# Performance work log

Hardware: AMD Instinct MI355X
Metric: run time of the kernel (lower is better)

## Reference

```python
import jax, jax.numpy as jnp
import numpy as np

NUM_HEADS = 8
WS = 7          # window size (hardcoded in source)
SR = 4          # sr_ratio
EPS = 1e-5


def _win_partition(t, ws, H, W):
    # t: [B, h, N, d] -> [B*h*nW, ws*ws, d]
    B, h, N, d = t.shape
    t = t.reshape(B * h, H // ws, ws, W // ws, ws, d)
    t = t.transpose(0, 1, 3, 2, 4, 5)
    return t.reshape(-1, ws * ws, d)


def _win_reverse(w, ws, H, W, h):
    # w: [B*h*nW, ws*ws, d] -> [B, H*W, h*d]
    d = w.shape[-1]
    Bh = w.shape[0] // ((H // ws) * (W // ws))
    x = w.reshape(Bh, H // ws, W // ws, ws, ws, d).transpose(0, 1, 3, 2, 4, 5)
    x = x.reshape(Bh // h, h, H, W, d).transpose(0, 2, 3, 1, 4)
    return x.reshape(Bh // h, H * W, h * d)


def setup_inputs() -> dict:
    key = jax.random.key(0)
    B, H, W, C = 32, 56, 56, 256
    N = H * W
    ks = jax.random.split(key, 10)
    s = lambda k, shp: jax.random.normal(k, shp, dtype=jnp.float32) * 0.02
    return {
        "x": jax.random.normal(ks[0], (B, N, C), dtype=jnp.float32),
        "lepe_lin_w": s(ks[1], (C, C)), "lepe_lin_b": jnp.zeros((C,), jnp.float32),
        "lepe_conv_w": s(ks[2], (3, 3, 1, C)), "lepe_conv_b": jnp.zeros((C,), jnp.float32),
        "sr_w": s(ks[3], (SR, SR, C, C)), "sr_b": jnp.zeros((C,), jnp.float32),
        "norm_g": jnp.ones((C,), jnp.float32), "norm_b": jnp.zeros((C,), jnp.float32),
        "q1_w": s(ks[4], (C, C // 2)), "kv1_w": s(ks[5], (C, C)),
        "q2_w": s(ks[6], (C, C // 2)), "kv2_w": s(ks[7], (C, C)),
        "proj_w": s(ks[8], (C, C)), "proj_b": jnp.zeros((C,), jnp.float32),
        "H": H, "W": W,
    }


def reference(x, lepe_lin_w, lepe_lin_b, lepe_conv_w, lepe_conv_b, sr_w, sr_b,
              norm_g, norm_b, q1_w, kv1_w, q2_w, kv2_w, proj_w, proj_b, H, W):
    B, N, C = x.shape
    h2 = NUM_HEADS // 2
    d = C // NUM_HEADS
    scale = d ** (-0.5)

    # lepe: linear -> depthwise 3x3 conv (NHWC) -> flatten back
    lep = (x @ lepe_lin_w + lepe_lin_b).reshape(B, H, W, C)
    lep = jax.lax.conv_general_dilated(
        lep, lepe_conv_w, window_strides=(1, 1), padding='SAME',
        dimension_numbers=('NHWC', 'HWIO', 'NHWC'), feature_group_count=C) + lepe_conv_b
    lepe = lep.reshape(B, N, C)

    # --- branch 1: global attention over sr-downsampled kv ---
    q1 = (x @ q1_w).reshape(B, N, h2, d).transpose(0, 2, 1, 3)         # [B,h2,N,d]
    img = x.reshape(B, H, W, C)
    x1_ = jax.lax.conv_general_dilated(
        img, sr_w, window_strides=(SR, SR), padding='VALID',
        dimension_numbers=('NHWC', 'HWIO', 'NHWC')) + sr_b              # [B,H/sr,W/sr,C]
    x1_ = x1_.reshape(B, -1, C)                                         # [B,N1,C]
    mu = jnp.mean(x1_, axis=-1, keepdims=True)
    var = jnp.mean(jnp.square(x1_ - mu), axis=-1, keepdims=True)
    x1_ = (x1_ - mu) * jax.lax.rsqrt(var + EPS) * norm_g + norm_b
    x1_ = jax.nn.gelu(x1_, approximate=False)
    kv1 = (x1_ @ kv1_w).reshape(B, -1, 2, h2, d).transpose(2, 0, 3, 1, 4)
    k1, v1 = kv1[0], kv1[1]                                             # [B,h2,N1,d]
    attn1 = jax.nn.softmax(jnp.einsum('bhnd,bhmd->bhnm', q1, k1) * scale, axis=-1)
    x1 = jnp.einsum('bhnm,bhmd->bhnd', attn1, v1)
    x1 = x1.transpose(0, 2, 1, 3).reshape(B, N, C // 2)

    # --- branch 2: 7x7 window attention ---
    q2 = (x @ q2_w).reshape(B, N, h2, d).transpose(0, 2, 1, 3)          # [B,h2,N,d]
    kv2 = (x @ kv2_w).reshape(B, -1, 2, h2, d).transpose(2, 0, 3, 1, 4)
    k2, v2 = kv2[0], kv2[1]
    q2w = _win_partition(q2, WS, H, W)                                  # [B*h2*nW,49,d]
    k2w = _win_partition(k2, WS, H, W)
    v2w = _win_partition(v2, WS, H, W)
    attn2 = jax.nn.softmax(jnp.einsum('wnd,wmd->wnm', q2w, k2w) * scale, axis=-1)
    x2w = jnp.einsum('wnm,wmd->wnd', attn2, v2w)
    x2 = _win_reverse(x2w, WS, H, W, h2)                                # [B,N,C/2]

    out = jnp.concatenate([x1, x2], axis=-1)
    out = (out + lepe) @ proj_w + proj_b
    return out
```

## Files before the change

kernel.cpp:

```cpp
#include <hip/hip_runtime.h>
#include <hip/hip_bf16.h>

typedef __hip_bfloat16 bf16;
typedef __attribute__((ext_vector_type(8))) short short8;
typedef __attribute__((ext_vector_type(4))) float floatx4;

__device__ __forceinline__ float toF(bf16 v){ return __bfloat162float(v); }
__device__ __forceinline__ float b2f(unsigned short u){
  return __uint_as_float(((unsigned int)u) << 16);
}
__device__ __forceinline__ unsigned short f2bu(float f){
  bf16 h = __float2bfloat16(f);
  return *(unsigned short*)&h;
}

__global__ __launch_bounds__(256) void prep_all_kernel(
    const float* __restrict__ x, bf16* __restrict__ xb,
    const float* __restrict__ sr_w, const float* __restrict__ lepe_w,
    const float* __restrict__ kv2_w, const float* __restrict__ q1_w,
    const float* __restrict__ q2_w, const float* __restrict__ kv1_w,
    const float* __restrict__ proj_w,
    bf16* __restrict__ wT_sr, bf16* __restrict__ wT_x,
    bf16* __restrict__ wT_kv1, bf16* __restrict__ wT_proj,
    int* __restrict__ srbase) {
  const int tid = threadIdx.x;
  if (blockIdx.x < 25088) {
    size_t i4 = ((size_t)blockIdx.x * 256 + tid) * 4;
    float4 v = *(const float4*)(x + i4);
    ushort4 o;
    o.x = f2bu(v.x); o.y = f2bu(v.y); o.z = f2bu(v.z); o.w = f2bu(v.w);
    *(ushort4*)(xb + i4) = o;
    return;
  }
  const int t = blockIdx.x - 25088;
  __shared__ float s[64][65];
  const float* src; bf16* dst; int K, N, kt, nt;
  if (t < 256)      { src = sr_w;   dst = wT_sr;          K = 4096; N = 256; kt = t >> 2;          nt = t & 3; }
  else if (t < 272) { src = lepe_w; dst = wT_x;           K = 256;  N = 256; kt = (t - 256) >> 2;  nt = (t - 256) & 3; }
  else if (t < 288) { src = kv2_w;  dst = wT_x + 65536;   K = 256;  N = 256; kt = (t - 272) >> 2;  nt = (t - 272) & 3; }
  else if (t < 296) { src = q1_w;   dst = wT_x + 131072;  K = 256;  N = 128; kt = (t - 288) >> 1;  nt = (t - 288) & 1; }
  else if (t < 304) { src = q2_w;   dst = wT_x + 163840;  K = 256;  N = 128; kt = (t - 296) >> 1;  nt = (t - 296) & 1; }
  else if (t < 320) { src = kv1_w;  dst = wT_kv1;         K = 256;  N = 256; kt = (t - 304) >> 2;  nt = (t - 304) & 3; }
  else if (t < 336) { src = proj_w; dst = wT_proj;        K = 256;  N = 256; kt = (t - 320) >> 2;  nt = (t - 320) & 3; }
  else {
    int tt = (t - 336) * 256 + tid;
    if (tt < 6272) {
      int b = tt / 196, p = tt - b * 196;
      int oy = p / 14, ox = p - oy * 14;
      srbase[tt] = ((b * 56 + oy * 4) * 56 + ox * 4) * 256;
    }
    return;
  }
  const int k0 = kt * 64, n0 = nt * 64;
#pragma unroll
  for (int p = tid; p < 4096; p += 256) {
    int k = p >> 6, n = p & 63;
    s[k][n] = src[(size_t)(k0 + k) * N + n0 + n];
  }
  __syncthreads();
#pragma unroll
  for (int p = tid; p < 4096; p += 256) {
    int n = p >> 6, k = p & 63;
    dst[(size_t)(n0 + n) * K + k0 + k] = __float2bfloat16(s[k][n]);
  }
}

__global__ __launch_bounds__(256) void gemm_x3(
    const bf16* __restrict__ A, const bf16* __restrict__ BT,
    const float* __restrict__ lepe_b,
    bf16* __restrict__ L1, bf16* __restrict__ KV2, bf16* __restrict__ Q12) {
  __shared__ uint4 As[128 * 5];
  __shared__ uint4 Bs[128 * 5];
  const int sw = (blockIdx.x & 7) * 588 + (blockIdx.x >> 3);
  const int bx = sw % 6, by = sw / 6;
  const int m0 = by * 128;
  const int n0 = bx * 128;
  const int tid = threadIdx.x;
  const int wave = tid >> 6, lane = tid & 63;
  const int wm = (wave >> 1) * 64, wn = (wave & 1) * 64;
  const int l15 = lane & 15, quad = lane >> 4;
  floatx4 zero = {0.f, 0.f, 0.f, 0.f};
  floatx4 acc[4][4];
#pragma unroll
  for (int i = 0; i < 4; i++)
#pragma unroll
    for (int j = 0; j < 4; j++) acc[i][j] = zero;

  for (int k0 = 0; k0 < 256; k0 += 32) {
#pragma unroll
    for (int it = 0; it < 2; it++) {
      int id = it * 256 + tid;
      int row = id >> 2, seg = id & 3;
      As[row * 5 + seg] = *(const uint4*)(A + (size_t)(m0 + row) * 256 + k0 + seg * 8);
      Bs[row * 5 + seg] = *(const uint4*)(BT + (size_t)(n0 + row) * 256 + k0 + seg * 8);
    }
    __syncthreads();
    short8 af[4], bfr[4];
#pragma unroll
    for (int i = 0; i < 4; i++)
      af[i] = *(const short8*)&As[(wm + i * 16 + l15) * 5 + quad];
#pragma unroll
    for (int j = 0; j < 4; j++)
      bfr[j] = *(const short8*)&Bs[(wn + j * 16 + l15) * 5 + quad];
#pragma unroll
    for (int i = 0; i < 4; i++)
#pragma unroll
      for (int j = 0; j < 4; j++)
        acc[i][j] = __builtin_amdgcn_mfma_f32_16x16x32_bf16(af[i], bfr[j], acc[i][j], 0, 0, 0);
    __syncthreads();
  }
  const int segN = n0 >> 8;
  bf16* Cd = (segN == 0) ? L1 : (segN == 1) ? KV2 : Q12;
  const int nc0 = n0 & 255;
#pragma unroll
  for (int j = 0; j < 4; j++) {
    int nl = nc0 + wn + j * 16 + l15;
    float bv = (segN == 0) ? lepe_b[nl] : 0.0f;
#pragma unroll
    for (int i = 0; i < 4; i++) {
      int m = m0 + wm + i * 16 + quad * 4;
#pragma unroll
      for (int r = 0; r < 4; r++)
        Cd[(size_t)(m + r) * 256 + nl] = __float2bfloat16(acc[i][j][r] + bv);
    }
  }
}

__global__ __launch_bounds__(256) void gemm_sr(
    const bf16* __restrict__ X, const bf16* __restrict__ BT,
    const int* __restrict__ base, float* __restrict__ C) {
  __shared__ uint4 As[128 * 5];
  __shared__ uint4 Bs[128 * 5];
  const int tid = threadIdx.x;
  const int m0 = blockIdx.y * 128;
  const int n0 = blockIdx.x * 128;
  const int kz = blockIdx.z;
  const int wave = tid >> 6, lane = tid & 63;
  const int wm = (wave >> 1) * 64, wn = (wave & 1) * 64;
  const int l15 = lane & 15, quad = lane >> 4;
  const int row0 = tid >> 2, row1 = 64 + (tid >> 2), seg = tid & 3;
  const int mb0 = base[m0 + row0];
  const int mb1 = base[m0 + row1];
  const bf16* bP0 = BT + (size_t)(n0 + row0) * 4096 + seg * 8;
  const bf16* bP1 = BT + (size_t)(n0 + row1) * 4096 + seg * 8;
  const int kbeg = kz * 512;
  floatx4 zero = {0.f, 0.f, 0.f, 0.f};
  floatx4 acc[4][4];
#pragma unroll
  for (int i = 0; i < 4; i++)
#pragma unroll
    for (int j = 0; j < 4; j++) acc[i][j] = zero;

  uint4 a0, a1, b0, b1;
  {
    int k = kbeg + seg * 8;
    int kp = k >> 8, c = k & 255;
    int off = ((kp >> 2) * 56 + (kp & 3)) * 256 + c;
    a0 = *(const uint4*)(X + (size_t)mb0 + off);
    a1 = *(const uint4*)(X + (size_t)mb1 + off);
    b0 = *(const uint4*)(bP0 + kbeg);
    b1 = *(const uint4*)(bP1 + kbeg);
  }
  for (int t = 0; t < 16; t++) {
    As[row0 * 5 + seg] = a0; As[row1 * 5 + seg] = a1;
    Bs[row0 * 5 + seg] = b0; Bs[row1 * 5 + seg] = b1;
    __syncthreads();
    if (t < 15) {
      int k = kbeg + (t + 1) * 32 + seg * 8;
      int kp = k >> 8, c = k & 255;
      int off = ((kp >> 2) * 56 + (kp & 3)) * 256 + c;
      a0 = *(const uint4*)(X + (size_t)mb0 + off);
      a1 = *(const uint4*)(X + (size_t)mb1 + off);
      b0 = *(const uint4*)(bP0 + kbeg + (t + 1) * 32);
      b1 = *(const uint4*)(bP1 + kbeg + (t + 1) * 32);
    }
    short8 af[4], bfr[4];
#pragma unroll
    for (int i = 0; i < 4; i++)
      af[i] = *(const short8*)&As[(wm + i * 16 + l15) * 5 + quad];
#pragma unroll
    for (int j = 0; j < 4; j++)
      bfr[j] = *(const short8*)&Bs[(wn + j * 16 + l15) * 5 + quad];
#pragma unroll
    for (int i = 0; i < 4; i++)
#pragma unroll
      for (int j = 0; j < 4; j++)
        acc[i][j] = __builtin_amdgcn_mfma_f32_16x16x32_bf16(bfr[j], af[i], acc[i][j], 0, 0, 0);
    __syncthreads();
  }
  float* Cp = C + (size_t)kz * (6272 * 256);
#pragma unroll
  for (int i = 0; i < 4; i++) {
    int m = m0 + wm + i * 16 + l15;
#pragma unroll
    for (int j = 0; j < 4; j++) {
      int nb = n0 + wn + j * 16 + quad * 4;
      float4 o = {acc[i][j][0], acc[i][j][1], acc[i][j][2], acc[i][j][3]};
      *(float4*)&Cp[(size_t)m * 256 + nb] = o;
    }
  }
}

__global__ __launch_bounds__(256) void gemm_kv1(
    const bf16* __restrict__ A, const bf16* __restrict__ BT,
    bf16* __restrict__ C) {
  __shared__ uint4 As[128 * 5];
  __shared__ uint4 Bs[128 * 5];
  const int tid = threadIdx.x;
  const int m0 = blockIdx.y * 128;
  const int n0 = blockIdx.x * 128;
  const int wave = tid >> 6, lane = tid & 63;
  const int wm = (wave >> 1) * 64, wn = (wave & 1) * 64;
  const int l15 = lane & 15, quad = lane >> 4;
  const int row0 = tid >> 2, row1 = 64 + (tid >> 2), seg = tid & 3;
  const bf16* aP0 = A + (size_t)(m0 + row0) * 256 + seg * 8;
  const bf16* aP1 = A + (size_t)(m0 + row1) * 256 + seg * 8;
  const bf16* bP0 = BT + (size_t)(n0 + row0) * 256 + seg * 8;
  const bf16* bP1 = BT + (size_t)(n0 + row1) * 256 + seg * 8;
  floatx4 zero = {0.f, 0.f, 0.f, 0.f};
  floatx4 acc[4][4];
#pragma unroll
  for (int i = 0; i < 4; i++)
#pragma unroll
    for (int j = 0; j < 4; j++) acc[i][j] = zero;

  uint4 a0 = *(const uint4*)aP0, a1 = *(const uint4*)aP1;
  uint4 b0 = *(const uint4*)bP0, b1 = *(const uint4*)bP1;
#pragma unroll
  for (int t = 0; t < 8; t++) {
    As[row0 * 5 + seg] = a0; As[row1 * 5 + seg] = a1;
    Bs[row0 * 5 + seg] = b0; Bs[row1 * 5 + seg] = b1;
    __syncthreads();
    if (t < 7) {
      int k0 = (t + 1) * 32;
      a0 = *(const uint4*)(aP0 + k0); a1 = *(const uint4*)(aP1 + k0);
      b0 = *(const uint4*)(bP0 + k0); b1 = *(const uint4*)(bP1 + k0);
    }
    short8 af[4], bfr[4];
#pragma unroll
    for (int i = 0; i < 4; i++)
      af[i] = *(const short8*)&As[(wm + i * 16 + l15) * 5 + quad];
#pragma unroll
    for (int j = 0; j < 4; j++)
      bfr[j] = *(const short8*)&Bs[(wn + j * 16 + l15) * 5 + quad];
#pragma unroll
    for (int i = 0; i < 4; i++)
#pragma unroll
      for (int j = 0; j < 4; j++)
        acc[i][j] = __builtin_amdgcn_mfma_f32_16x16x32_bf16(bfr[j], af[i], acc[i][j], 0, 0, 0);
    __syncthreads();
  }
#pragma unroll
  for (int i = 0; i < 4; i++) {
    int m = m0 + wm + i * 16 + l15;
#pragma unroll
    for (int j = 0; j < 4; j++) {
      int nb = n0 + wn + j * 16 + quad * 4;
      ushort4 o;
      o.x = f2bu(acc[i][j][0]); o.y = f2bu(acc[i][j][1]);
      o.z = f2bu(acc[i][j][2]); o.w = f2bu(acc[i][j][3]);
      *(ushort4*)&C[(size_t)m * 256 + nb] = o;
    }
  }
}

__global__ __launch_bounds__(256) void gemm_proj_mfma(
    const bf16* __restrict__ X1, const bf16* __restrict__ X2,
    const bf16* __restrict__ L2, const bf16* __restrict__ BT,
    const float* __restrict__ bias, float* __restrict__ C) {
  __shared__ uint4 As[128 * 5];
  __shared__ uint4 Bs[128 * 5];
  const int sw = (blockIdx.x & 7) * 196 + (blockIdx.x >> 3);
  const int tid = threadIdx.x;
  const int m0 = (sw >> 1) * 128;
  const int n0 = (sw & 1) * 128;
  const int wave = tid >> 6, lane = tid & 63;
  const int wm = (wave >> 1) * 64, wn = (wave & 1) * 64;
  const int l15 = lane & 15, quad = lane >> 4;
  const int row0 = tid >> 2, row1 = 64 + (tid >> 2), seg = tid & 3;
  const bf16* bP0 = BT + (size_t)(n0 + row0) * 256 + seg * 8;
  const bf16* bP1 = BT + (size_t)(n0 + row1) * 256 + seg * 8;
  floatx4 zero = {0.f, 0.f, 0.f, 0.f};
  floatx4 acc[4][4];
#pragma unroll
  for (int i = 0; i < 4; i++)
#pragma unroll
    for (int j = 0; j < 4; j++) acc[i][j] = zero;

  uint4 va0, va1, vl0, vl1, b0, b1;
  {
    int k = seg * 8;
    const bf16* s0 = X1 + (size_t)(m0 + row0) * 128 + k;
    const bf16* s1 = X1 + (size_t)(m0 + row1) * 128 + k;
    va0 = *(const uint4*)s0; va1 = *(const uint4*)s1;
    vl0 = *(const uint4*)(L2 + (size_t)(m0 + row0) * 256 + k);
    vl1 = *(const uint4*)(L2 + (size_t)(m0 + row1) * 256 + k);
    b0 = *(const uint4*)bP0; b1 = *(const uint4*)bP1;
  }
#pragma unroll
  for (int t = 0; t < 8; t++) {
    {
      unsigned short o0[8], o1[8];
      const unsigned short* pa0 = (const unsigned short*)&va0;
      const unsigned short* pl0 = (const unsigned short*)&vl0;
      const unsigned short* pa1 = (const unsigned short*)&va1;
      const unsigned short* pl1 = (const unsigned short*)&vl1;
#pragma unroll
      for (int e = 0; e < 8; e++) {
        o0[e] = f2bu(b2f(pa0[e]) + b2f(pl0[e]));
        o1[e] = f2bu(b2f(pa1[e]) + b2f(pl1[e]));
      }
      As[row0 * 5 + seg] = *(const uint4*)o0;
      As[row1 * 5 + seg] = *(const uint4*)o1;
      Bs[row0 * 5 + seg] = b0;
      Bs[row1 * 5 + seg] = b1;
    }
    __syncthreads();
    if (t < 7) {
      int k = (t + 1) * 32 + seg * 8;
      const bf16* s0 = (k < 128) ? X1 + (size_t)(m0 + row0) * 128 + k
                                 : X2 + (size_t)(m0 + row0) * 128 + (k - 128);
      const bf16* s1 = (k < 128) ? X1 + (size_t)(m0 + row1) * 128 + k
                                 : X2 + (size_t)(m0 + row1) * 128 + (k - 128);
      va0 = *(const uint4*)s0; va1 = *(const uint4*)s1;
      vl0 = *(const uint4*)(L2 + (size_t)(m0 + row0) * 256 + k);
      vl1 = *(const uint4*)(L2 + (size_t)(m0 + row1) * 256 + k);
      b0 = *(const uint4*)(bP0 + (t + 1) * 32);
      b1 = *(const uint4*)(bP1 + (t + 1) * 32);
    }
    short8 af[4], bfr[4];
#pragma unroll
    for (int i = 0; i < 4; i++)
      af[i] = *(const short8*)&As[(wm + i * 16 + l15) * 5 + quad];
#pragma unroll
    for (int j = 0; j < 4; j++)
      bfr[j] = *(const short8*)&Bs[(wn + j * 16 + l15) * 5 + quad];
#pragma unroll
    for (int i = 0; i < 4; i++)
#pragma unroll
      for (int j = 0; j < 4; j++)
        acc[i][j] = __builtin_amdgcn_mfma_f32_16x16x32_bf16(bfr[j], af[i], acc[i][j], 0, 0, 0);
    __syncthreads();
  }
#pragma unroll
  for (int i = 0; i < 4; i++) {
    int m = m0 + wm + i * 16 + l15;
#pragma unroll
    for (int j = 0; j < 4; j++) {
      int nb = n0 + wn + j * 16 + quad * 4;
      float4 bv = *(const float4*)&bias[nb];
      float4 o = {acc[i][j][0] + bv.x, acc[i][j][1] + bv.y,
                  acc[i][j][2] + bv.z, acc[i][j][3] + bv.w};
      *(float4*)&C[(size_t)m * 256 + nb] = o;
    }
  }
}

__global__ __launch_bounds__(256) void dwconv8_kernel(
    const bf16* __restrict__ in, const float* __restrict__ w,
    const float* __restrict__ bias, bf16* __restrict__ out) {
  const int idx = blockIdx.x * 256 + threadIdx.x;
  const int c8 = (idx & 31) * 8;
  const int sp = idx >> 5;
  const int xx = sp % 56;
  const int yb = sp / 56;
  const int yy = yb % 56;
  const int b  = yb / 56;
  float4 bb0 = *(const float4*)&bias[c8];
  float4 bb1 = *(const float4*)&bias[c8 + 4];
  float acc[8] = {bb0.x, bb0.y, bb0.z, bb0.w, bb1.x, bb1.y, bb1.z, bb1.w};
#pragma unroll
  for (int dy = 0; dy < 3; dy++) {
    int y = yy + dy - 1;
    if ((unsigned)y >= 56u) continue;
#pragma unroll
    for (int dx = 0; dx < 3; dx++) {
      int x = xx + dx - 1;
      if ((unsigned)x >= 56u) continue;
      uint4 v = *(const uint4*)&in[((size_t)((b * 56 + y) * 56 + x)) * 256 + c8];
      const unsigned short* pv = (const unsigned short*)&v;
      float4 w0 = *(const float4*)&w[(dy * 3 + dx) * 256 + c8];
      float4 w1 = *(const float4*)&w[(dy * 3 + dx) * 256 + c8 + 4];
      float wf[8] = {w0.x, w0.y, w0.z, w0.w, w1.x, w1.y, w1.z, w1.w};
#pragma unroll
      for (int e = 0; e < 8; e++) acc[e] += b2f(pv[e]) * wf[e];
    }
  }
  unsigned short o[8];
#pragma unroll
  for (int e = 0; e < 8; e++) o[e] = f2bu(acc[e]);
  *(uint4*)&out[(size_t)sp * 256 + c8] = *(const uint4*)o;
}

__global__ __launch_bounds__(256) void ln_gelu_kernel(
    const float* __restrict__ in, const float* __restrict__ srb,
    const float* __restrict__ g, const float* __restrict__ bb,
    bf16* __restrict__ out) {
  const int tok = blockIdx.x;
  const int tid = threadIdx.x;
  float v = srb[tid];
  const float* p = in + (size_t)tok * 256 + tid;
#pragma unroll
  for (int c = 0; c < 8; c++) v += p[(size_t)c * 1605632];
  float s = v, s2 = v * v;
#pragma unroll
  for (int o = 32; o > 0; o >>= 1) {
    s += __shfl_down(s, o, 64);
    s2 += __shfl_down(s2, o, 64);
  }
  __shared__ float rs[4], rs2[4];
  int wid = tid >> 6, lane = tid & 63;
  if (lane == 0) { rs[wid] = s; rs2[wid] = s2; }
  __syncthreads();
  float tot = rs[0] + rs[1] + rs[2] + rs[3];
  float tot2 = rs2[0] + rs2[1] + rs2[2] + rs2[3];
  float mean = tot * (1.0f / 256.0f);
  float var = tot2 * (1.0f / 256.0f) - mean * mean;
  float y = (v - mean) * rsqrtf(var + 1e-5f) * g[tid] + bb[tid];
  out[(size_t)tok * 256 + tid] =
      __float2bfloat16(0.5f * y * (1.0f + erff(y * 0.70710678118654752f)));
}

__global__ __launch_bounds__(256) void attn1_mfma(
    const bf16* __restrict__ Q12, const bf16* __restrict__ KV,
    bf16* __restrict__ O) {
  __shared__ bf16 sk[224 * 32];
  __shared__ bf16 svT[32 * 232];
  __shared__ bf16 pbuf[4][64 * 32];
  const int b = blockIdx.z, h = blockIdx.y, chunk = blockIdx.x;
  const int tid = threadIdx.x;
  const int wave = tid >> 6, lane = tid & 63;
  const int l15 = lane & 15, quad = lane >> 4;
  for (int i = tid; i < 224 * 4; i += 256) {
    int m = i >> 2, c = i & 3;
    uint4 kv4 = {0u, 0u, 0u, 0u}, vv4 = {0u, 0u, 0u, 0u};
    if (m < 196) {
      const bf16* p = KV + ((size_t)(b * 196 + m)) * 256 + h * 32 + c * 8;
      kv4 = *(const uint4*)p;
      vv4 = *(const uint4*)(p + 128);
    }
    *(uint4*)&sk[m * 32 + c * 8] = kv4;
    const unsigned short* pv = (const unsigned short*)&vv4;
#pragma unroll
    for (int e = 0; e < 8; e++)
      *(unsigned short*)&svT[(c * 8 + e) * 232 + m] = pv[e];
  }
  __syncthreads();
  const int q0 = chunk * 256 + wave * 64;
  short8 aq[4];
#pragma unroll
  for (int i = 0; i < 4; i++) {
    int qr = q0 + i * 16 + l15; if (qr > 3135) qr = 3135;
    aq[i] = *(const short8*)(Q12 + ((size_t)(b * 3136 + qr)) * 256 + h * 32 + quad * 8);
  }
  const float scale = 0.17677669529663687f;
  floatx4 zero = {0.f, 0.f, 0.f, 0.f};
  floatx4 acc[4][2];
  float lsum[4][4];
#pragma unroll
  for (int i = 0; i < 4; i++) {
    acc[i][0] = zero; acc[i][1] = zero;
#pragma unroll
    for (int r = 0; r < 4; r++) lsum[i][r] = 0.f;
  }
  bf16* pw = pbuf[wave];
  for (int c = 0; c < 7; c++) {
    const int kv0 = c * 32;
    short8 bk[2];
#pragma unroll
    for (int n = 0; n < 2; n++)
      bk[n] = *(const short8*)&sk[(kv0 + n * 16 + l15) * 32 + quad * 8];
    floatx4 s[4][2];
#pragma unroll
    for (int i = 0; i < 4; i++)
#pragma unroll
      for (int n = 0; n < 2; n++)
        s[i][n] = __builtin_amdgcn_mfma_f32_16x16x32_bf16(aq[i], bk[n], zero, 0, 0, 0);
#pragma unroll
    for (int i = 0; i < 4; i++)
#pragma unroll
      for (int n = 0; n < 2; n++) {
        bool valid = (kv0 + n * 16 + l15) < 196;
#pragma unroll
        for (int r = 0; r < 4; r++) {
          float p = valid ? __expf(s[i][n][r] * scale) : 0.f;
          lsum[i][r] += p;
          pw[(i * 16 + quad * 4 + r) * 32 + n * 16 + l15] = __float2bfloat16(p);
        }
      }
    asm volatile("s_waitcnt lgkmcnt(0)" ::: "memory");
    short8 ap[4], bv[2];
#pragma unroll
    for (int i = 0; i < 4; i++)
      ap[i] = *(const short8*)&pw[(i * 16 + l15) * 32 + quad * 8];
#pragma unroll
    for (int n = 0; n < 2; n++)
      bv[n] = *(const short8*)&svT[(n * 16 + l15) * 232 + kv0 + quad * 8];
#pragma unroll
    for (int i = 0; i < 4; i++)
#pragma unroll
      for (int n = 0; n < 2; n++)
        acc[i][n] = __builtin_amdgcn_mfma_f32_16x16x32_bf16(ap[i], bv[n], acc[i][n], 0, 0, 0);
  }
#pragma unroll
  for (int i = 0; i < 4; i++)
#pragma unroll
    for (int r = 0; r < 4; r++) {
      float v = lsum[i][r];
      v += __shfl_xor(v, 1, 64);
      v += __shfl_xor(v, 2, 64);
      v += __shfl_xor(v, 4, 64);
      v += __shfl_xor(v, 8, 64);
      lsum[i][r] = 1.0f / v;
    }
#pragma unroll
  for (int i = 0; i < 4; i++)
#pragma unroll
    for (int r = 0; r < 4; r++) {
      int qr = q0 + i * 16 + quad * 4 + r;
      if (qr < 3136) {
        bf16* op = O + ((size_t)(b * 3136 + qr)) * 128 + h * 32;
        op[l15]      = __float2bfloat16(acc[i][0][r] * lsum[i][r]);
        op[16 + l15] = __float2bfloat16(acc[i][1][r] * lsum[i][r]);
      }
    }
}

__global__ __launch_bounds__(256) void attn2_mfma(
    const bf16* __restrict__ Q12, const bf16* __restrict__ KV2,
    bf16* __restrict__ O) {
  __shared__ bf16 sk[64 * 136];
  __shared__ bf16 pb[4][64 * 72];
  const int b = blockIdx.y;
  const int win = blockIdx.x;
  const int wy = win >> 3, wx = win & 7;
  const int tid = threadIdx.x;
  const int wave = tid >> 6, lane = tid & 63;
  const int l15 = lane & 15, quad = lane >> 4;
  const int h = wave;

  for (int i = tid; i < 49 * 16; i += 256) {
    int m = i >> 4, c = i & 15;
    int iy = m / 7, ix = m - iy * 7;
    int n = (wy * 7 + iy) * 56 + wx * 7 + ix;
    *(uint4*)&sk[m * 136 + c * 8] =
        *(const uint4*)&KV2[((size_t)(b * 3136 + n)) * 256 + c * 8];
  }

  short8 bvv[2][2];
#pragma unroll
  for (int ks = 0; ks < 2; ks++)
#pragma unroll
    for (int nt = 0; nt < 2; nt++)
#pragma unroll
      for (int e = 0; e < 8; e++) {
        int k = ks * 32 + quad * 8 + e; if (k > 48) k = 48;
        int iy = k / 7, ix = k - iy * 7;
        int n = (wy * 7 + iy) * 56 + wx * 7 + ix;
        bvv[ks][nt][e] = ((const short*)KV2)[((size_t)(b * 3136 + n)) * 256
                                             + 128 + h * 32 + nt * 16 + l15];
      }

  short8 aq[4];
#pragma unroll
  for (int i = 0; i < 4; i++) {
    int lq = i * 16 + l15; if (lq > 48) lq = 48;
    int iy = lq / 7, ix = lq - iy * 7;
    int n = (wy * 7 + iy) * 56 + wx * 7 + ix;
    aq[i] = *(const short8*)(Q12 + ((size_t)(b * 3136 + n)) * 256 + 128 + h * 32 + quad * 8);
  }
  __syncthreads();

  const float scale = 0.17677669529663687f;
  floatx4 zero = {0.f, 0.f, 0.f, 0.f};
  floatx4 acc[4][2];
  float lsum[4][4];
#pragma unroll
  for (int i = 0; i < 4; i++) {
    acc[i][0] = zero; acc[i][1] = zero;
#pragma unroll
    for (int r = 0; r < 4; r++) lsum[i][r] = 0.f;
  }
  bf16* pw = pb[wave];
#pragma unroll
  for (int c = 0; c < 2; c++) {
    const int kv0 = c * 32;
    short8 bk[2];
#pragma unroll
    for (int n = 0; n < 2; n++)
      bk[n] = *(const short8*)&sk[(kv0 + n * 16 + l15) * 136 + h * 32 + quad * 8];
    floatx4 s[4][2];
#pragma unroll
    for (int i = 0; i < 4; i++)
#pragma unroll
      for (int n = 0; n < 2; n++)
        s[i][n] = __builtin_amdgcn_mfma_f32_16x16x32_bf16(aq[i], bk[n], zero, 0, 0, 0);
#pragma unroll
    for (int i = 0; i < 4; i++)
#pragma unroll
      for (int n = 0; n < 2; n++) {
        bool valid = (kv0 + n * 16 + l15) < 49;
#pragma unroll
        for (int r = 0; r < 4; r++) {
          float p = valid ? __expf(s[i][n][r] * scale) : 0.f;
          lsum[i][r] += p;
          pw[(i * 16 + quad * 4 + r) * 72 + kv0 + n * 16 + l15] = __float2bfloat16(p);
        }
      }
  }
  asm volatile("s_waitcnt lgkmcnt(0)" ::: "memory");
#pragma unroll
  for (int ks = 0; ks < 2; ks++) {
    short8 ap[4];
#pragma unroll
    for (int i = 0; i < 4; i++)
      ap[i] = *(const short8*)&pw[(i * 16 + l15) * 72 + ks * 32 + quad * 8];
#pragma unroll
    for (int i = 0; i < 4; i++)
#pragma unroll
      for (int nt = 0; nt < 2; nt++)
        acc[i][nt] = __builtin_amdgcn_mfma_f32_16x16x32_bf16(ap[i], bvv[ks][nt], acc[i][nt], 0, 0, 0);
  }
#pragma unroll
  for (int i = 0; i < 4; i++)
#pragma unroll
    for (int r = 0; r < 4; r++) {
      float v = lsum[i][r];
      v += __shfl_xor(v, 1, 64);
      v += __shfl_xor(v, 2, 64);
      v += __shfl_xor(v, 4, 64);
      v += __shfl_xor(v, 8, 64);
      lsum[i][r] = 1.0f / v;
    }
#pragma unroll
  for (int i = 0; i < 4; i++)
#pragma unroll
    for (int r = 0; r < 4; r++) {
      int lq = i * 16 + quad * 4 + r;
      if (lq < 49) {
        int iy = lq / 7, ix = lq - iy * 7;
        int n = (wy * 7 + iy) * 56 + wx * 7 + ix;
        bf16* op = O + ((size_t)(b * 3136 + n)) * 128 + h * 32;
        op[l15]      = __float2bfloat16(acc[i][0][r] * lsum[i][r]);
        op[16 + l15] = __float2bfloat16(acc[i][1][r] * lsum[i][r]);
      }
    }
}

extern "C" void kernel_launch(void* const* d_in, const int* in_sizes, int n_in,
                              void* d_out, int out_size, void* d_ws, size_t ws_size,
                              hipStream_t stream) {
  const float* x           = (const float*)d_in[0];
  const float* lepe_lin_w  = (const float*)d_in[1];
  const float* lepe_lin_b  = (const float*)d_in[2];
  const float* lepe_conv_w = (const float*)d_in[3];
  const float* lepe_conv_b = (const float*)d_in[4];
  const float* sr_w        = (const float*)d_in[5];
  const float* sr_b        = (const float*)d_in[6];
  const float* norm_g      = (const float*)d_in[7];
  const float* norm_b      = (const float*)d_in[8];
  const float* q1_w        = (const float*)d_in[9];
  const float* kv1_w       = (const float*)d_in[10];
  const float* q2_w        = (const float*)d_in[11];
  const float* kv2_w       = (const float*)d_in[12];
  const float* proj_w      = (const float*)d_in[13];
  const float* proj_b      = (const float*)d_in[14];
  float* out = (float*)d_out;

  char* ws = (char*)d_ws;
  char* ob = (char*)d_out;
  const size_t szBNC = 100352ull * 256 * 2;
  const size_t szBNh = 100352ull * 128 * 2;
  bf16*  xb  = (bf16*)ob;
  bf16*  Q12 = (bf16*)(ob + szBNC);
  bf16*  L1  = (bf16*)ws;
  float* X1Ppart = (float*)ws;
  bf16*  X1N = (bf16*)ob;
  bf16*  KV1 = (bf16*)(ob + 8388608);
  bf16*  X1  = (bf16*)ws;
  bf16*  L2  = (bf16*)(ws + szBNC);
  bf16*  X2  = (bf16*)(ws + 2 * szBNC);
  char*  wtb = ws + 2 * szBNC + szBNh;
  bf16* wT_x    = (bf16*)(wtb);
  bf16* wT_kv1  = (bf16*)(wtb + 393216);
  bf16* wT_proj = (bf16*)(wtb + 524288);
  bf16* wT_sr   = (bf16*)(wtb + 655360);
  int*  srbase  = (int*)(wtb + 655360 + 2097152);
  bf16* KV2     = (bf16*)(wtb + 655360 + 2097152 + 32768);

  prep_all_kernel<<<25449, 256, 0, stream>>>(
      x, xb, sr_w, lepe_lin_w, kv2_w, q1_w, q2_w, kv1_w, proj_w,
      wT_sr, wT_x, wT_kv1, wT_proj, srbase);

  gemm_x3<<<4704, 256, 0, stream>>>(xb, wT_x, lepe_lin_b, L1, KV2, Q12);

  dwconv8_kernel<<<12544, 256, 0, stream>>>(L1, lepe_conv_w, lepe_conv_b, L2);

  attn2_mfma<<<dim3(64, 32), 256, 0, stream>>>(Q12, KV2, X2);

  gemm_sr<<<dim3(2, 49, 8), 256, 0, stream>>>(xb, wT_sr, srbase, X1Ppart);
  ln_gelu_kernel<<<6272, 256, 0, stream>>>(X1Ppart, sr_b, norm_g, norm_b, X1N);
  gemm_kv1<<<dim3(2, 49), 256, 0, stream>>>(X1N, wT_kv1, KV1);
  attn1_mfma<<<dim3(13, 4, 32), 256, 0, stream>>>(Q12, KV1, X1);

  gemm_proj_mfma<<<1568, 256, 0, stream>>>(
      X1, X2, L2, wT_proj, proj_b, out);
}
```

Measured before the change: 520.6 us.

## Merge independent kernels into combined launches with block-index dispatch

Folds the sr-conv GEMM into the x-projection GEMM launch, the depthwise conv with the LayerNorm+GELU, and the window attention with the kv1 GEMM, dispatching on blockIdx ranges. The sr split-K is cut from 8 to 4 slices, so each block runs a longer K loop and the LN kernel sums 4 partials instead of 8. The goal is to remove launch gaps and small-grid tail underutilisation by running independent work concurrently. In exchange, the combined kernels share one register and LDS budget, which may lower occupancy, and the workspace buffers are reassigned so X1Ppart now overlaps X2.

Result: faster. 479.2 us, median of 2 (-8.0%).

```diff
diff --git a/kernel.cpp b/kernel.cpp
--- a/kernel.cpp
+++ b/kernel.cpp
@@ -65,16 +65,14 @@
   }
 }
 
-__global__ __launch_bounds__(256) void gemm_x3(
-    const bf16* __restrict__ A, const bf16* __restrict__ BT,
+__global__ __launch_bounds__(256) void gemm_x3sr(
+    const bf16* __restrict__ A, const bf16* __restrict__ BTx,
     const float* __restrict__ lepe_b,
-    bf16* __restrict__ L1, bf16* __restrict__ KV2, bf16* __restrict__ Q12) {
+    bf16* __restrict__ L1, bf16* __restrict__ KV2, bf16* __restrict__ Q12,
+    const bf16* __restrict__ BTsr, const int* __restrict__ base,
+    float* __restrict__ Cpart) {
   __shared__ uint4 As[128 * 5];
   __shared__ uint4 Bs[128 * 5];
-  const int sw = (blockIdx.x & 7) * 588 + (blockIdx.x >> 3);
-  const int bx = sw % 6, by = sw / 6;
-  const int m0 = by * 128;
-  const int n0 = bx * 128;
   const int tid = threadIdx.x;
   const int wave = tid >> 6, lane = tid & 63;
   const int wm = (wave >> 1) * 64, wn = (wave & 1) * 64;
@@ -86,182 +84,462 @@
 #pragma unroll
     for (int j = 0; j < 4; j++) acc[i][j] = zero;
 
-  for (int k0 = 0; k0 < 256; k0 += 32) {
-#pragma unroll
-    for (int it = 0; it < 2; it++) {
-      int id = it * 256 + tid;
-      int row = id >> 2, seg = id & 3;
-      As[row * 5 + seg] = *(const uint4*)(A + (size_t)(m0 + row) * 256 + k0 + seg * 8);
-      Bs[row * 5 + seg] = *(const uint4*)(BT + (size_t)(n0 + row) * 256 + k0 + seg * 8);
-    }
-    __syncthreads();
-    short8 af[4], bfr[4];
-#pragma unroll
-    for (int i = 0; i < 4; i++)
-      af[i] = *(const short8*)&As[(wm + i * 16 + l15) * 5 + quad];
-#pragma unroll
-    for (int j = 0; j < 4; j++)
-      bfr[j] = *(const short8*)&Bs[(wn + j * 16 + l15) * 5 + quad];
-#pragma unroll
-    for (int i = 0; i < 4; i++)
-#pragma unroll
-      for (int j = 0; j < 4; j++)
-        acc[i][j] = __builtin_amdgcn_mfma_f32_16x16x32_bf16(af[i], bfr[j], acc[i][j], 0, 0, 0);
-    __syncthreads();
-  }
-  const int segN = n0 >> 8;
-  bf16* Cd = (segN == 0) ? L1 : (segN == 1) ? KV2 : Q12;
-  const int nc0 = n0 & 255;
-#pragma unroll
-  for (int j = 0; j < 4; j++) {
-    int nl = nc0 + wn + j * 16 + l15;
-    float bv = (segN == 0) ? lepe_b[nl] : 0.0f;
-#pragma unroll
-    for (int i = 0; i < 4; i++) {
-      int m = m0 + wm + i * 16 + quad * 4;
-#pragma unroll
-      for (int r = 0; r < 4; r++)
-        Cd[(size_t)(m + r) * 256 + nl] = __float2bfloat16(acc[i][j][r] + bv);
-    }
-  }
-}
-
-__global__ __launch_bounds__(256) void gemm_sr(
-    const bf16* __restrict__ X, const bf16* __restrict__ BT,
-    const int* __restrict__ base, float* __restrict__ C) {
-  __shared__ uint4 As[128 * 5];
-  __shared__ uint4 Bs[128 * 5];
-  const int tid = threadIdx.x;
-  const int m0 = blockIdx.y * 128;
-  const int n0 = blockIdx.x * 128;
-  const int kz = blockIdx.z;
-  const int wave = tid >> 6, lane = tid & 63;
-  const int wm = (wave >> 1) * 64, wn = (wave & 1) * 64;
-  const int l15 = lane & 15, quad = lane >> 4;
-  const int row0 = tid >> 2, row1 = 64 + (tid >> 2), seg = tid & 3;
-  const int mb0 = base[m0 + row0];
-  const int mb1 = base[m0 + row1];
-  const bf16* bP0 = BT + (size_t)(n0 + row0) * 4096 + seg * 8;
-  const bf16* bP1 = BT + (size_t)(n0 + row1) * 4096 + seg * 8;
-  const int kbeg = kz * 512;
-  floatx4 zero = {0.f, 0.f, 0.f, 0.f};
-  floatx4 acc[4][4];
-#pragma unroll
-  for (int i = 0; i < 4; i++)
-#pragma unroll
-    for (int j = 0; j < 4; j++) acc[i][j] = zero;
-
-  uint4 a0, a1, b0, b1;
-  {
-    int k = kbeg + seg * 8;
-    int kp = k >> 8, c = k & 255;
-    int off = ((kp >> 2) * 56 + (kp & 3)) * 256 + c;
-    a0 = *(const uint4*)(X + (size_t)mb0 + off);
-    a1 = *(const uint4*)(X + (size_t)mb1 + off);
-    b0 = *(const uint4*)(bP0 + kbeg);
-    b1 = *(const uint4*)(bP1 + kbeg);
-  }
-  for (int t = 0; t < 16; t++) {
-    As[row0 * 5 + seg] = a0; As[row1 * 5 + seg] = a1;
-    Bs[row0 * 5 + seg] = b0; Bs[row1 * 5 + seg] = b1;
-    __syncthreads();
-    if (t < 15) {
-      int k = kbeg + (t + 1) * 32 + seg * 8;
+  if (blockIdx.x < 392) {
+    const int r = blockIdx.x;
+    const int kz = r / 98, rem = r - kz * 98;
+    const int m0 = (rem >> 1) * 128;
+    const int n0 = (rem & 1) * 128;
+    const int row0 = tid >> 2, row1 = 64 + (tid >> 2), seg = tid & 3;
+    const int mb0 = base[m0 + row0];
+    const int mb1 = base[m0 + row1];
+    const bf16* bP0 = BTsr + (size_t)(n0 + row0) * 4096 + seg * 8;
+    const bf16* bP1 = BTsr + (size_t)(n0 + row1) * 4096 + seg * 8;
+    const int kbeg = kz * 1024;
+    uint4 a0, a1, b0, b1;
+    {
+      int k = kbeg + seg * 8;
       int kp = k >> 8, c = k & 255;
       int off = ((kp >> 2) * 56 + (kp & 3)) * 256 + c;
-      a0 = *(const uint4*)(X + (size_t)mb0 + off);
-      a1 = *(const uint4*)(X + (size_t)mb1 + off);
-      b0 = *(const uint4*)(bP0 + kbeg + (t + 1) * 32);
-      b1 = *(const uint4*)(bP1 + kbeg + (t + 1) * 32);
-    }
-    short8 af[4], bfr[4];
-#pragma unroll
-    for (int i = 0; i < 4; i++)
-      af[i] = *(const short8*)&As[(wm + i * 16 + l15) * 5 + quad];
-#pragma unroll
-    for (int j = 0; j < 4; j++)
-      bfr[j] = *(const short8*)&Bs[(wn + j * 16 + l15) * 5 + quad];
-#pragma unroll
-    for (int i = 0; i < 4; i++)
+      a0 = *(const uint4*)(A + (size_t)mb0 + off);
+      a1 = *(const uint4*)(A + (size_t)mb1 + off);
+      b0 = *(const uint4*)(bP0 + kbeg);
+      b1 = *(const uint4*)(bP1 + kbeg);
+    }
+    for (int t = 0; t < 32; t++) {
+      As[row0 * 5 + seg] = a0; As[row1 * 5 + seg] = a1;
+      Bs[row0 * 5 + seg] = b0; Bs[row1 * 5 + seg] = b1;
+      __syncthreads();
+      if (t < 31) {
+        int k = kbeg + (t + 1) * 32 + seg * 8;
+        int kp = k >> 8, c = k & 255;
+        int off = ((kp >> 2) * 56 + (kp & 3)) * 256 + c;
+        a0 = *(const uint4*)(A + (size_t)mb0 + off);
+        a1 = *(const uint4*)(A + (size_t)mb1 + off);
+        b0 = *(const uint4*)(bP0 + kbeg + (t + 1) * 32);
+        b1 = *(const uint4*)(bP1 + kbeg + (t + 1) * 32);
+      }
+      short8 af[4], bfr[4];
+#pragma unroll
+      for (int i = 0; i < 4; i++)
+        af[i] = *(const short8*)&As[(wm + i * 16 + l15) * 5 + quad];
 #pragma unroll
       for (int j = 0; j < 4; j++)
-        acc[i][j] = __builtin_amdgcn_mfma_f32_16x16x32_bf16(bfr[j], af[i], acc[i][j], 0, 0, 0);
+        bfr[j] = *(const short8*)&Bs[(wn + j * 16 + l15) * 5 + quad];
+#pragma unroll
+      for (int i = 0; i < 4; i++)
+#pragma unroll
+        for (int j = 0; j < 4; j++)
+          acc[i][j] = __builtin_amdgcn_mfma_f32_16x16x32_bf16(bfr[j], af[i], acc[i][j], 0, 0, 0);
+      __syncthreads();
+    }
+    float* Cp = Cpart + (size_t)kz * (6272 * 256);
+#pragma unroll
+    for (int i = 0; i < 4; i++) {
+      int m = m0 + wm + i * 16 + l15;
+#pragma unroll
+      for (int j = 0; j < 4; j++) {
+        int nb = n0 + wn + j * 16 + quad * 4;
+        float4 o = {acc[i][j][0], acc[i][j][1], acc[i][j][2], acc[i][j][3]};
+        *(float4*)&Cp[(size_t)m * 256 + nb] = o;
+      }
+    }
+  } else {
+    const int bid = blockIdx.x - 392;
+    const int sw = (bid & 7) * 588 + (bid >> 3);
+    const int bx = sw % 6, by = sw / 6;
+    const int m0 = by * 128;
+    const int n0 = bx * 128;
+    for (int k0 = 0; k0 < 256; k0 += 32) {
+#pragma unroll
+      for (int it = 0; it < 2; it++) {
+        int id = it * 256 + tid;
+        int row = id >> 2, seg = id & 3;
+        As[row * 5 + seg] = *(const uint4*)(A + (size_t)(m0 + row) * 256 + k0 + seg * 8);
+        Bs[row * 5 + seg] = *(const uint4*)(BTx + (size_t)(n0 + row) * 256 + k0 + seg * 8);
+      }
+      __syncthreads();
+      short8 af[4], bfr[4];
+#pragma unroll
+      for (int i = 0; i < 4; i++)
+        af[i] = *(const short8*)&As[(wm + i * 16 + l15) * 5 + quad];
+#pragma unroll
+      for (int j = 0; j < 4; j++)
+        bfr[j] = *(const short8*)&Bs[(wn + j * 16 + l15) * 5 + quad];
+#pragma unroll
+      for (int i = 0; i < 4; i++)
+#pragma unroll
+        for (int j = 0; j < 4; j++)
+          acc[i][j] = __builtin_amdgcn_mfma_f32_16x16x32_bf16(af[i], bfr[j], acc[i][j], 0, 0, 0);
+      __syncthreads();
+    }
+    const int segN = n0 >> 8;
+    bf16* Cd = (segN == 0) ? L1 : (segN == 1) ? KV2 : Q12;
+    const int nc0 = n0 & 255;
+#pragma unroll
+    for (int j = 0; j < 4; j++) {
+      int nl = nc0 + wn + j * 16 + l15;
+      float bv = (segN == 0) ? lepe_b[nl] : 0.0f;
+#pragma unroll
+      for (int i = 0; i < 4; i++) {
+        int m = m0 + wm + i * 16 + quad * 4;
+#pragma unroll
+        for (int r = 0; r < 4; r++)
+          Cd[(size_t)(m + r) * 256 + nl] = __float2bfloat16(acc[i][j][r] + bv);
+      }
+    }
+  }
+}
+
+__global__ __launch_bounds__(256) void dwln_kernel(
+    const bf16* __restrict__ L1in, const float* __restrict__ w,
+    const float* __restrict__ cb,
+    const float* __restrict__ part, const float* __restrict__ srb,
+    const float* __restrict__ g, const float* __restrict__ bb,
+    bf16* __restrict__ L2out, bf16* __restrict__ X1Nout) {
+  const int tid = threadIdx.x;
+  __shared__ float rs[4], rs2[4];
+  if (blockIdx.x < 12544) {
+    const int idx = blockIdx.x * 256 + tid;
+    const int c8 = (idx & 31) * 8;
+    const int sp = idx >> 5;
+    const int xx = sp % 56;
+    const int yb = sp / 56;
+    const int yy = yb % 56;
+    const int b  = yb / 56;
+    float4 bb0 = *(const float4*)&cb[c8];
+    float4 bb1 = *(const float4*)&cb[c8 + 4];
+    float acc[8] = {bb0.x, bb0.y, bb0.z, bb0.w, bb1.x, bb1.y, bb1.z, bb1.w};
+#pragma unroll
+    for (int dy = 0; dy < 3; dy++) {
+      int y = yy + dy - 1;
+      if ((unsigned)y >= 56u) continue;
+#pragma unroll
+      for (int dx = 0; dx < 3; dx++) {
+        int x = xx + dx - 1;
+        if ((unsigned)x >= 56u) continue;
+        uint4 v = *(const uint4*)&L1in[((size_t)((b * 56 + y) * 56 + x)) * 256 + c8];
+        const unsigned short* pv = (const unsigned short*)&v;
+        float4 w0 = *(const float4*)&w[(dy * 3 + dx) * 256 + c8];
+        float4 w1 = *(const float4*)&w[(dy * 3 + dx) * 256 + c8 + 4];
+        float wf[8] = {w0.x, w0.y, w0.z, w0.w, w1.x, w1.y, w1.z, w1.w};
+#pragma unroll
+        for (int e = 0; e < 8; e++) acc[e] += b2f(pv[e]) * wf[e];
+      }
+    }
+    unsigned short o[8];
+#pragma unroll
+    for (int e = 0; e < 8; e++) o[e] = f2bu(acc[e]);
+    *(uint4*)&L2out[(size_t)sp * 256 + c8] = *(const uint4*)o;
+  } else {
+    const int tok = blockIdx.x - 12544;
+    float v = srb[tid];
+    const float* p = part + (size_t)tok * 256 + tid;
+#pragma unroll
+    for (int c = 0; c < 4; c++) v += p[(size_t)c * 1605632];
+    float s = v, s2 = v * v;
+#pragma unroll
+    for (int o = 32; o > 0; o >>= 1) {
+      s += __shfl_down(s, o, 64);
+      s2 += __shfl_down(s2, o, 64);
+    }
+    int wid = tid >> 6, lane = tid & 63;
+    if (lane == 0) { rs[wid] = s; rs2[wid] = s2; }
     __syncthreads();
-  }
-  float* Cp = C + (size_t)kz * (6272 * 256);
+    float tot = rs[0] + rs[1] + rs[2] + rs[3];
+    float tot2 = rs2[0] + rs2[1] + rs2[2] + rs2[3];
+    float mean = tot * (1.0f / 256.0f);
+    float var = tot2 * (1.0f / 256.0f) - mean * mean;
+    float y = (v - mean) * rsqrtf(var + 1e-5f) * g[tid] + bb[tid];
+    X1Nout[(size_t)tok * 256 + tid] =
+        __float2bfloat16(0.5f * y * (1.0f + erff(y * 0.70710678118654752f)));
+  }
+}
+
+__global__ __launch_bounds__(256) void attn2kv1_kernel(
+    const bf16* __restrict__ Q12, const bf16* __restrict__ KV2,
+    const bf16* __restrict__ X1N, const bf16* __restrict__ wT_kv1,
+    bf16* __restrict__ X2, bf16* __restrict__ KV1) {
+  __shared__ __align__(16) char smem[54272];
+  const int tid = threadIdx.x;
+  const int wave = tid >> 6, lane = tid & 63;
+  const int l15 = lane & 15, quad = lane >> 4;
+  floatx4 zero = {0.f, 0.f, 0.f, 0.f};
+
+  if (blockIdx.x < 2048) {
+    bf16* sk = (bf16*)smem;
+    bf16* pbAll = (bf16*)(smem + 17408);
+    const int b = blockIdx.x >> 6;
+    const int win = blockIdx.x & 63;
+    const int wy = win >> 3, wx = win & 7;
+    const int h = wave;
+
+    for (int i = tid; i < 49 * 16; i += 256) {
+      int m = i >> 4, c = i & 15;
+      int iy = m / 7, ix = m - iy * 7;
+      int n = (wy * 7 + iy) * 56 + wx * 7 + ix;
+      *(uint4*)&sk[m * 136 + c * 8] =
+          *(const uint4*)&KV2[((size_t)(b * 3136 + n)) * 256 + c * 8];
+    }
+
+    short8 bvv[2][2];
+#pragma unroll
+    for (int ks = 0; ks < 2; ks++)
+#pragma unroll
+      for (int nt = 0; nt < 2; nt++)
+#pragma unroll
+        for (int e = 0; e < 8; e++) {
+          int k = ks * 32 + quad * 8 + e; if (k > 48) k = 48;
+          int iy = k / 7, ix = k - iy * 7;
+          int n = (wy * 7 + iy) * 56 + wx * 7 + ix;
+          bvv[ks][nt][e] = ((const short*)KV2)[((size_t)(b * 3136 + n)) * 256
+                                               + 128 + h * 32 + nt * 16 + l15];
+        }
+
+    short8 aq[4];
+#pragma unroll
+    for (int i = 0; i < 4; i++) {
+      int lq = i * 16 + l15; if (lq > 48) lq = 48;
+      int iy = lq / 7, ix = lq - iy * 7;
+      int n = (wy * 7 + iy) * 56 + wx * 7 + ix;
+      aq[i] = *(const short8*)(Q12 + ((size_t)(b * 3136 + n)) * 256 + 128 + h * 32 + quad * 8);
+    }
+    __syncthreads();
+
+    const float scale = 0.17677669529663687f;
+    floatx4 acc[4][2];
+    float lsum[4][4];
+#pragma unroll
+    for (int i = 0; i < 4; i++) {
+      acc[i][0] = zero; acc[i][1] = zero;
+#pragma unroll
+      for (int r = 0; r < 4; r++) lsum[i][r] = 0.f;
+    }
+    bf16* pw = pbAll + wave * (64 * 72);
+#pragma unroll
+    for (int c = 0; c < 2; c++) {
+      const int kv0 = c * 32;
+      short8 bk[2];
+#pragma unroll
+      for (int n = 0; n < 2; n++)
+        bk[n] = *(const short8*)&sk[(kv0 + n * 16 + l15) * 136 + h * 32 + quad * 8];
+      floatx4 s[4][2];
+#pragma unroll
+      for (int i = 0; i < 4; i++)
+#pragma unroll
+        for (int n = 0; n < 2; n++)
+          s[i][n] = __builtin_amdgcn_mfma_f32_16x16x32_bf16(aq[i], bk[n], zero, 0, 0, 0);
+#pragma unroll
+      for (int i = 0; i < 4; i++)
+#pragma unroll
+        for (int n = 0; n < 2; n++) {
+          bool valid = (kv0 + n * 16 + l15) < 49;
+#pragma unroll
+          for (int r = 0; r < 4; r++) {
+            float p = valid ? __expf(s[i][n][r] * scale) : 0.f;
+            lsum[i][r] += p;
+            pw[(i * 16 + quad * 4 + r) * 72 + kv0 + n * 16 + l15] = __float2bfloat16(p);
+          }
+        }
+    }
+    asm volatile("s_waitcnt lgkmcnt(0)" ::: "memory");
+#pragma unroll
+    for (int ks = 0; ks < 2; ks++) {
+      short8 ap[4];
+#pragma unroll
+      for (int i = 0; i < 4; i++)
+        ap[i] = *(const short8*)&pw[(i * 16 + l15) * 72 + ks * 32 + quad * 8];
+#pragma unroll
+      for (int i = 0; i < 4; i++)
+#pragma unroll
+        for (int nt = 0; nt < 2; nt++)
+          acc[i][nt] = __builtin_amdgcn_mfma_f32_16x16x32_bf16(ap[i], bvv[ks][nt], acc[i][nt], 0, 0, 0);
+    }
+#pragma unroll
+    for (int i = 0; i < 4; i++)
+#pragma unroll
+      for (int r = 0; r < 4; r++) {
+        float v = lsum[i][r];
+        v += __shfl_xor(v, 1, 64);
+        v += __shfl_xor(v, 2, 64);
+        v += __shfl_xor(v, 4, 64);
+        v += __shfl_xor(v, 8, 64);
+        lsum[i][r] = 1.0f / v;
+      }
+#pragma unroll
+    for (int i = 0; i < 4; i++)
+#pragma unroll
+      for (int r = 0; r < 4; r++) {
+        int lq = i * 16 + quad * 4 + r;
+        if (lq < 49) {
+          int iy = lq / 7, ix = lq - iy * 7;
+          int n = (wy * 7 + iy) * 56 + wx * 7 + ix;
+          bf16* op = X2 + ((size_t)(b * 3136 + n)) * 128 + h * 32;
+          op[l15]      = __float2bfloat16(acc[i][0][r] * lsum[i][r]);
+          op[16 + l15] = __float2bfloat16(acc[i][1][r] * lsum[i][r]);
+        }
+      }
+  } else {
+    uint4* As = (uint4*)smem;
+    uint4* Bs = (uint4*)(smem + 10240);
+    const int r = blockIdx.x - 2048;
+    const int m0 = (r >> 1) * 128;
+    const int n0 = (r & 1) * 128;
+    const int wm = (wave >> 1) * 64, wn = (wave & 1) * 64;
+    const int row0 = tid >> 2, row1 = 64 + (tid >> 2), seg = tid & 3;
+    const bf16* aP0 = X1N + (size_t)(m0 + row0) * 256 + seg * 8;
+    const bf16* aP1 = X1N + (size_t)(m0 + row1) * 256 + seg * 8;
+    const bf16* bP0 = wT_kv1 + (size_t)(n0 + row0) * 256 + seg * 8;
+    const bf16* bP1 = wT_kv1 + (size_t)(n0 + row1) * 256 + seg * 8;
+    floatx4 acc[4][4];
+#pragma unroll
+    for (int i = 0; i < 4; i++)
+#pragma unroll
+      for (int j = 0; j < 4; j++) acc[i][j] = zero;
+
+    uint4 a0 = *(const uint4*)aP0, a1 = *(const uint4*)aP1;
+    uint4 b0 = *(const uint4*)bP0, b1 = *(const uint4*)bP1;
+#pragma unroll
+    for (int t = 0; t < 8; t++) {
+      As[row0 * 5 + seg] = a0; As[row1 * 5 + seg] = a1;
+      Bs[row0 * 5 + seg] = b0; Bs[row1 * 5 + seg] = b1;
+      __syncthreads();
+      if (t < 7) {
+        int k0 = (t + 1) * 32;
+        a0 = *(const uint4*)(aP0 + k0); a1 = *(const uint4*)(aP1 + k0);
+        b0 = *(const uint4*)(bP0 + k0); b1 = *(const uint4*)(bP1 + k0);
+      }
+      short8 af[4], bfr[4];
+#pragma unroll
+      for (int i = 0; i < 4; i++)
+        af[i] = *(const short8*)&As[(wm + i * 16 + l15) * 5 + quad];
+#pragma unroll
+      for (int j = 0; j < 4; j++)
+        bfr[j] = *(const short8*)&Bs[(wn + j * 16 + l15) * 5 + quad];
+#pragma unroll
+      for (int i = 0; i < 4; i++)
+#pragma unroll
+        for (int j = 0; j < 4; j++)
+          acc[i][j] = __builtin_amdgcn_mfma_f32_16x16x32_bf16(bfr[j], af[i], acc[i][j], 0, 0, 0);
+      __syncthreads();
+    }
+#pragma unroll
+    for (int i = 0; i < 4; i++) {
+      int m = m0 + wm + i * 16 + l15;
+#pragma unroll
+      for (int j = 0; j < 4; j++) {
+        int nb = n0 + wn + j * 16 + quad * 4;
+        ushort4 o;
+        o.x = f2bu(acc[i][j][0]); o.y = f2bu(acc[i][j][1]);
+        o.z = f2bu(acc[i][j][2]); o.w = f2bu(acc[i][j][3]);
+        *(ushort4*)&KV1[(size_t)m * 256 + nb] = o;
+      }
+    }
+  }
+}
+
+__global__ __launch_bounds__(256) void attn1_mfma(
+    const bf16* __restrict__ Q12, const bf16* __restrict__ KV,
+    bf16* __restrict__ O) {
+  __shared__ bf16 sk[224 * 32];
+  __shared__ bf16 svT[32 * 232];
+  __shared__ bf16 pbuf[4][64 * 32];
+  const int b = blockIdx.z, h = blockIdx.y, chunk = blockIdx.x;
+  const int tid = threadIdx.x;
+  const int wave = tid >> 6, lane = tid & 63;
+  const int l15 = lane & 15, quad = lane >> 4;
+  for (int i = tid; i < 224 * 4; i += 256) {
+    int m = i >> 2, c = i & 3;
+    uint4 kv4 = {0u, 0u, 0u, 0u}, vv4 = {0u, 0u, 0u, 0u};
+    if (m < 196) {
+      const bf16* p = KV + ((size_t)(b * 196 + m)) * 256 + h * 32 + c * 8;
+      kv4 = *(const uint4*)p;
+      vv4 = *(const uint4*)(p + 128);
+    }
+    *(uint4*)&sk[m * 32 + c * 8] = kv4;
+    const unsigned short* pv = (const unsigned short*)&vv4;
+#pragma unroll
+    for (int e = 0; e < 8; e++)
+      *(unsigned short*)&svT[(c * 8 + e) * 232 + m] = pv[e];
+  }
+  __syncthreads();
+  const int q0 = chunk * 256 + wave * 64;
+  short8 aq[4];
 #pragma unroll
   for (int i = 0; i < 4; i++) {
-    int m = m0 + wm + i * 16 + l15;
-#pragma unroll
-    for (int j = 0; j < 4; j++) {
-      int nb = n0 + wn + j * 16 + quad * 4;
-      float4 o = {acc[i][j][0], acc[i][j][1], acc[i][j][2], acc[i][j][3]};
-      *(float4*)&Cp[(size_t)m * 256 + nb] = o;
-    }
-  }
-}
-
-__global__ __launch_bounds__(256) void gemm_kv1(
-    const bf16* __restrict__ A, const bf16* __restrict__ BT,
-    bf16* __restrict__ C) {
-  __shared__ uint4 As[128 * 5];
-  __shared__ uint4 Bs[128 * 5];
-  const int tid = threadIdx.x;
-  const int m0 = blockIdx.y * 128;
-  const int n0 = blockIdx.x * 128;
-  const int wave = tid >> 6, lane = tid & 63;
-  const int wm = (wave >> 1) * 64, wn = (wave & 1) * 64;
-  const int l15 = lane & 15, quad = lane >> 4;
-  const int row0 = tid >> 2, row1 = 64 + (tid >> 2), seg = tid & 3;
-  const bf16* aP0 = A + (size_t)(m0 + row0) * 256 + seg * 8;
-  const bf16* aP1 = A + (size_t)(m0 + row1) * 256 + seg * 8;
-  const bf16* bP0 = BT + (size_t)(n0 + row0) * 256 + seg * 8;
-  const bf16* bP1 = BT + (size_t)(n0 + row1) * 256 + seg * 8;
+    int qr = q0 + i * 16 + l15; if (qr > 3135) qr = 3135;
+    aq[i] = *(const short8*)(Q12 + ((size_t)(b * 3136 + qr)) * 256 + h * 32 + quad * 8);
+  }
+  const float scale = 0.17677669529663687f;
   floatx4 zero = {0.f, 0.f, 0.f, 0.f};
-  floatx4 acc[4][4];
+  floatx4 acc[4][2];
+  float lsum[4][4];
+#pragma unroll
+  for (int i = 0; i < 4; i++) {
+    acc[i][0] = zero; acc[i][1] = zero;
+#pragma unroll
+    for (int r = 0; r < 4; r++) lsum[i][r] = 0.f;
+  }
+  bf16* pw = pbuf[wave];
+  for (int c = 0; c < 7; c++) {
+    const int kv0 = c * 32;
+    short8 bk[2];
+#pragma unroll
+    for (int n = 0; n < 2; n++)
+      bk[n] = *(const short8*)&sk[(kv0 + n * 16 + l15) * 32 + quad * 8];
+    floatx4 s[4][2];
+#pragma unroll
+    for (int i = 0; i < 4; i++)
+#pragma unroll
+      for (int n = 0; n < 2; n++)
+        s[i][n] = __builtin_amdgcn_mfma_f32_16x16x32_bf16(aq[i], bk[n], zero, 0, 0, 0);
+#pragma unroll
+    for (int i = 0; i < 4; i++)
+#pragma unroll
+      for (int n = 0; n < 2; n++) {
+        bool valid = (kv0 + n * 16 + l15) < 196;
+#pragma unroll
+        for (int r = 0; r < 4; r++) {
+          float p = valid ? __expf(s[i][n][r] * scale) : 0.f;
+          lsum[i][r] += p;
+          pw[(i * 16 + quad * 4 + r) * 32 + n * 16 + l15] = __float2bfloat16(p);
+        }
+      }
+    asm volatile("s_waitcnt lgkmcnt(0)" ::: "memory");
+    short8 ap[4], bv[2];
+#pragma unroll
+    for (int i = 0; i < 4; i++)
+      ap[i] = *(const short8*)&pw[(i * 16 + l15) * 32 + quad * 8];
+#pragma unroll
+    for (int n = 0; n < 2; n++)
+      bv[n] = *(const short8*)&svT[(n * 16 + l15) * 232 + kv0 + quad * 8];
+#pragma unroll
+    for (int i = 0; i < 4; i++)
+#pragma unroll
+      for (int n = 0; n < 2; n++)
+        acc[i][n] = __builtin_amdgcn_mfma_f32_16x16x32_bf16(ap[i], bv[n], acc[i][n], 0, 0, 0);
+  }
 #pragma unroll
   for (int i = 0; i < 4; i++)
 #pragma unroll
-    for (int j = 0; j < 4; j++) acc[i][j] = zero;
-
-  uint4 a0 = *(const uint4*)aP0, a1 = *(const uint4*)aP1;
-  uint4 b0 = *(const uint4*)bP0, b1 = *(const uint4*)bP1;
-#pragma unroll
-  for (int t = 0; t < 8; t++) {
-    As[row0 * 5 + seg] = a0; As[row1 * 5 + seg] = a1;
-    Bs[row0 * 5 + seg] = b0; Bs[row1 * 5 + seg] = b1;
-    __syncthreads();
-    if (t < 7) {
-      int k0 = (t + 1) * 32;
-      a0 = *(const uint4*)(aP0 + k0); a1 = *(const uint4*)(aP1 + k0);
-      b0 = *(const uint4*)(bP0 + k0); b1 = *(const uint4*)(bP1 + k0);
-    }
-    short8 af[4], bfr[4];
-#pragma unroll
-    for (int i = 0; i < 4; i++)
-      af[i] = *(const short8*)&As[(wm + i * 16 + l15) * 5 + quad];
-#pragma unroll
-    for (int j = 0; j < 4; j++)
-      bfr[j] = *(const short8*)&Bs[(wn + j * 16 + l15) * 5 + quad];
-#pragma unroll
-    for (int i = 0; i < 4; i++)
-#pragma unroll
-      for (int j = 0; j < 4; j++)
-        acc[i][j] = __builtin_amdgcn_mfma_f32_16x16x32_bf16(bfr[j], af[i], acc[i][j], 0, 0, 0);
-    __syncthreads();
-  }
-#pragma unroll
-  for (int i = 0; i < 4; i++) {
-    int m = m0 + wm + i * 16 + l15;
-#pragma unroll
-    for (int j = 0; j < 4; j++) {
-      int nb = n0 + wn + j * 16 + quad * 4;
-      ushort4 o;
-      o.x = f2bu(acc[i][j][0]); o.y = f2bu(acc[i][j][1]);
-      o.z = f2bu(acc[i][j][2]); o.w = f2bu(acc[i][j][3]);
-      *(ushort4*)&C[(size_t)m * 256 + nb] = o;
-    }
-  }
+    for (int r = 0; r < 4; r++) {
+      float v = lsum[i][r];
+      v += __shfl_xor(v, 1, 64);
+      v += __shfl_xor(v, 2, 64);
+      v += __shfl_xor(v, 4, 64);
+      v += __shfl_xor(v, 8, 64);
+      lsum[i][r] = 1.0f / v;
+    }
+#pragma unroll
+  for (int i = 0; i < 4; i++)
+#pragma unroll
+    for (int r = 0; r < 4; r++) {
+      int qr = q0 + i * 16 + quad * 4 + r;
+      if (qr < 3136) {
+        bf16* op = O + ((size_t)(b * 3136 + qr)) * 128 + h * 32;
+        op[l15]      = __float2bfloat16(acc[i][0][r] * lsum[i][r]);
+        op[16 + l15] = __float2bfloat16(acc[i][1][r] * lsum[i][r]);
+      }
+    }
 }
 
 __global__ __launch_bounds__(256) void gemm_proj_mfma(
@@ -354,297 +632,6 @@
       *(float4*)&C[(size_t)m * 256 + nb] = o;
     }
   }
-}
-
-__global__ __launch_bounds__(256) void dwconv8_kernel(
-    const bf16* __restrict__ in, const float* __restrict__ w,
-    const float* __restrict__ bias, bf16* __restrict__ out) {
-  const int idx = blockIdx.x * 256 + threadIdx.x;
-  const int c8 = (idx & 31) * 8;
-  const int sp = idx >> 5;
-  const int xx = sp % 56;
-  const int yb = sp / 56;
-  const int yy = yb % 56;
-  const int b  = yb / 56;
-  float4 bb0 = *(const float4*)&bias[c8];
-  float4 bb1 = *(const float4*)&bias[c8 + 4];
-  float acc[8] = {bb0.x, bb0.y, bb0.z, bb0.w, bb1.x, bb1.y, bb1.z, bb1.w};
-#pragma unroll
-  for (int dy = 0; dy < 3; dy++) {
-    int y = yy + dy - 1;
-    if ((unsigned)y >= 56u) continue;
-#pragma unroll
-    for (int dx = 0; dx < 3; dx++) {
-      int x = xx + dx - 1;
-      if ((unsigned)x >= 56u) continue;
-      uint4 v = *(const uint4*)&in[((size_t)((b * 56 + y) * 56 + x)) * 256 + c8];
-      const unsigned short* pv = (const unsigned short*)&v;
-      float4 w0 = *(const float4*)&w[(dy * 3 + dx) * 256 + c8];
-      float4 w1 = *(const float4*)&w[(dy * 3 + dx) * 256 + c8 + 4];
-      float wf[8] = {w0.x, w0.y, w0.z, w0.w, w1.x, w1.y, w1.z, w1.w};
-#pragma unroll
-      for (int e = 0; e < 8; e++) acc[e] += b2f(pv[e]) * wf[e];
-    }
-  }
-  unsigned short o[8];
-#pragma unroll
-  for (int e = 0; e < 8; e++) o[e] = f2bu(acc[e]);
-  *(uint4*)&out[(size_t)sp * 256 + c8] = *(const uint4*)o;
-}
-
-__global__ __launch_bounds__(256) void ln_gelu_kernel(
-    const float* __restrict__ in, const float* __restrict__ srb,
-    const float* __restrict__ g, const float* __restrict__ bb,
-    bf16* __restrict__ out) {
-  const int tok = blockIdx.x;
-  const int tid = threadIdx.x;
-  float v = srb[tid];
-  const float* p = in + (size_t)tok * 256 + tid;
-#pragma unroll
-  for (int c = 0; c < 8; c++) v += p[(size_t)c * 1605632];
-  float s = v, s2 = v * v;
-#pragma unroll
-  for (int o = 32; o > 0; o >>= 1) {
-    s += __shfl_down(s, o, 64);
-    s2 += __shfl_down(s2, o, 64);
-  }
-  __shared__ float rs[4], rs2[4];
-  int wid = tid >> 6, lane = tid & 63;
-  if (lane == 0) { rs[wid] = s; rs2[wid] = s2; }
-  __syncthreads();
-  float tot = rs[0] + rs[1] + rs[2] + rs[3];
-  float tot2 = rs2[0] + rs2[1] + rs2[2] + rs2[3];
-  float mean = tot * (1.0f / 256.0f);
-  float var = tot2 * (1.0f / 256.0f) - mean * mean;
-  float y = (v - mean) * rsqrtf(var + 1e-5f) * g[tid] + bb[tid];
-  out[(size_t)tok * 256 + tid] =
-      __float2bfloat16(0.5f * y * (1.0f + erff(y * 0.70710678118654752f)));
-}
-
-__global__ __launch_bounds__(256) void attn1_mfma(
-    const bf16* __restrict__ Q12, const bf16* __restrict__ KV,
-    bf16* __restrict__ O) {
-  __shared__ bf16 sk[224 * 32];
-  __shared__ bf16 svT[32 * 232];
-  __shared__ bf16 pbuf[4][64 * 32];
-  const int b = blockIdx.z, h = blockIdx.y, chunk = blockIdx.x;
-  const int tid = threadIdx.x;
-  const int wave = tid >> 6, lane = tid & 63;
-  const int l15 = lane & 15, quad = lane >> 4;
-  for (int i = tid; i < 224 * 4; i += 256) {
-    int m = i >> 2, c = i & 3;
-    uint4 kv4 = {0u, 0u, 0u, 0u}, vv4 = {0u, 0u, 0u, 0u};
-    if (m < 196) {
-      const bf16* p = KV + ((size_t)(b * 196 + m)) * 256 + h * 32 + c * 8;
-      kv4 = *(const uint4*)p;
-      vv4 = *(const uint4*)(p + 128);
-    }
-    *(uint4*)&sk[m * 32 + c * 8] = kv4;
-    const unsigned short* pv = (const unsigned short*)&vv4;
-#pragma unroll
-    for (int e = 0; e < 8; e++)
-      *(unsigned short*)&svT[(c * 8 + e) * 232 + m] = pv[e];
-  }
-  __syncthreads();
-  const int q0 = chunk * 256 + wave * 64;
-  short8 aq[4];
-#pragma unroll
-  for (int i = 0; i < 4; i++) {
-    int qr = q0 + i * 16 + l15; if (qr > 3135) qr = 3135;
-    aq[i] = *(const short8*)(Q12 + ((size_t)(b * 3136 + qr)) * 256 + h * 32 + quad * 8);
-  }
-  const float scale = 0.17677669529663687f;
-  floatx4 zero = {0.f, 0.f, 0.f, 0.f};
-  floatx4 acc[4][2];
-  float lsum[4][4];
-#pragma unroll
-  for (int i = 0; i < 4; i++) {
-    acc[i][0] = zero; acc[i][1] = zero;
-#pragma unroll
-    for (int r = 0; r < 4; r++) lsum[i][r] = 0.f;
-  }
-  bf16* pw = pbuf[wave];
-  for (int c = 0; c < 7; c++) {
-    const int kv0 = c * 32;
-    short8 bk[2];
-#pragma unroll
-    for (int n = 0; n < 2; n++)
-      bk[n] = *(const short8*)&sk[(kv0 + n * 16 + l15) * 32 + quad * 8];
-    floatx4 s[4][2];
-#pragma unroll
-    for (int i = 0; i < 4; i++)
-#pragma unroll
-      for (int n = 0; n < 2; n++)
-        s[i][n] = __builtin_amdgcn_mfma_f32_16x16x32_bf16(aq[i], bk[n], zero, 0, 0, 0);
-#pragma unroll
-    for (int i = 0; i < 4; i++)
-#pragma unroll
-      for (int n = 0; n < 2; n++) {
-        bool valid = (kv0 + n * 16 + l15) < 196;
-#pragma unroll
-        for (int r = 0; r < 4; r++) {
-          float p = valid ? __expf(s[i][n][r] * scale) : 0.f;
-          lsum[i][r] += p;
-          pw[(i * 16 + quad * 4 + r) * 32 + n * 16 + l15] = __float2bfloat16(p);
-        }
-      }
-    asm volatile("s_waitcnt lgkmcnt(0)" ::: "memory");
-    short8 ap[4], bv[2];
-#pragma unroll
-    for (int i = 0; i < 4; i++)
-      ap[i] = *(const short8*)&pw[(i * 16 + l15) * 32 + quad * 8];
-#pragma unroll
-    for (int n = 0; n < 2; n++)
-      bv[n] = *(const short8*)&svT[(n * 16 + l15) * 232 + kv0 + quad * 8];
-#pragma unroll
-    for (int i = 0; i < 4; i++)
-#pragma unroll
-      for (int n = 0; n < 2; n++)
-        acc[i][n] = __builtin_amdgcn_mfma_f32_16x16x32_bf16(ap[i], bv[n], acc[i][n], 0, 0, 0);
-  }
-#pragma unroll
-  for (int i = 0; i < 4; i++)
-#pragma unroll
-    for (int r = 0; r < 4; r++) {
-      float v = lsum[i][r];
-      v += __shfl_xor(v, 1, 64);
-      v += __shfl_xor(v, 2, 64);
-      v += __shfl_xor(v, 4, 64);
-      v += __shfl_xor(v, 8, 64);
-      lsum[i][r] = 1.0f / v;
-    }
-#pragma unroll
-  for (int i = 0; i < 4; i++)
-#pragma unroll
-    for (int r = 0; r < 4; r++) {
-      int qr = q0 + i * 16 + quad * 4 + r;
-      if (qr < 3136) {
-        bf16* op = O + ((size_t)(b * 3136 + qr)) * 128 + h * 32;
-        op[l15]      = __float2bfloat16(acc[i][0][r] * lsum[i][r]);
-        op[16 + l15] = __float2bfloat16(acc[i][1][r] * lsum[i][r]);
-      }
-    }
-}
-
-__global__ __launch_bounds__(256) void attn2_mfma(
-    const bf16* __restrict__ Q12, const bf16* __restrict__ KV2,
-    bf16* __restrict__ O) {
-  __shared__ bf16 sk[64 * 136];
-  __shared__ bf16 pb[4][64 * 72];
-  const int b = blockIdx.y;
-  const int win = blockIdx.x;
-  const int wy = win >> 3, wx = win & 7;
-  const int tid = threadIdx.x;
-  const int wave = tid >> 6, lane = tid & 63;
-  const int l15 = lane & 15, quad = lane >> 4;
-  const int h = wave;
-
-  for (int i = tid; i < 49 * 16; i += 256) {
-    int m = i >> 4, c = i & 15;
-    int iy = m / 7, ix = m - iy * 7;
-    int n = (wy * 7 + iy) * 56 + wx * 7 + ix;
-    *(uint4*)&sk[m * 136 + c * 8] =
-        *(const uint4*)&KV2[((size_t)(b * 3136 + n)) * 256 + c * 8];
-  }
-
-  short8 bvv[2][2];
-#pragma unroll
-  for (int ks = 0; ks < 2; ks++)
-#pragma unroll
-    for (int nt = 0; nt < 2; nt++)
-#pragma unroll
-      for (int e = 0; e < 8; e++) {
-        int k = ks * 32 + quad * 8 + e; if (k > 48) k = 48;
-        int iy = k / 7, ix = k - iy * 7;
-        int n = (wy * 7 + iy) * 56 + wx * 7 + ix;
-        bvv[ks][nt][e] = ((const short*)KV2)[((size_t)(b * 3136 + n)) * 256
-                                             + 128 + h * 32 + nt * 16 + l15];
-      }
-
-  short8 aq[4];
-#pragma unroll
-  for (int i = 0; i < 4; i++) {
-    int lq = i * 16 + l15; if (lq > 48) lq = 48;
-    int iy = lq / 7, ix = lq - iy * 7;
-    int n = (wy * 7 + iy) * 56 + wx * 7 + ix;
-    aq[i] = *(const short8*)(Q12 + ((size_t)(b * 3136 + n)) * 256 + 128 + h * 32 + quad * 8);
-  }
-  __syncthreads();
-
-  const float scale = 0.17677669529663687f;
-  floatx4 zero = {0.f, 0.f, 0.f, 0.f};
-  floatx4 acc[4][2];
-  float lsum[4][4];
-#pragma unroll
-  for (int i = 0; i < 4; i++) {
-    acc[i][0] = zero; acc[i][1] = zero;
-#pragma unroll
-    for (int r = 0; r < 4; r++) lsum[i][r] = 0.f;
-  }
-  bf16* pw = pb[wave];
-#pragma unroll
-  for (int c = 0; c < 2; c++) {
-    const int kv0 = c * 32;
-    short8 bk[2];
-#pragma unroll
-    for (int n = 0; n < 2; n++)
-      bk[n] = *(const short8*)&sk[(kv0 + n * 16 + l15) * 136 + h * 32 + quad * 8];
-    floatx4 s[4][2];
-#pragma unroll
-    for (int i = 0; i < 4; i++)
-#pragma unroll
-      for (int n = 0; n < 2; n++)
-        s[i][n] = __builtin_amdgcn_mfma_f32_16x16x32_bf16(aq[i], bk[n], zero, 0, 0, 0);
-#pragma unroll
-    for (int i = 0; i < 4; i++)
-#pragma unroll
-      for (int n = 0; n < 2; n++) {
-        bool valid = (kv0 + n * 16 + l15) < 49;
-#pragma unroll
-        for (int r = 0; r < 4; r++) {
-          float p = valid ? __expf(s[i][n][r] * scale) : 0.f;
-          lsum[i][r] += p;
-          pw[(i * 16 + quad * 4 + r) * 72 + kv0 + n * 16 + l15] = __float2bfloat16(p);
-        }
-      }
-  }
-  asm volatile("s_waitcnt lgkmcnt(0)" ::: "memory");
-#pragma unroll
-  for (int ks = 0; ks < 2; ks++) {
-    short8 ap[4];
-#pragma unroll
-    for (int i = 0; i < 4; i++)
-      ap[i] = *(const short8*)&pw[(i * 16 + l15) * 72 + ks * 32 + quad * 8];
-#pragma unroll
-    for (int i = 0; i < 4; i++)
-#pragma unroll
-      for (int nt = 0; nt < 2; nt++)
-        acc[i][nt] = __builtin_amdgcn_mfma_f32_16x16x32_bf16(ap[i], bvv[ks][nt], acc[i][nt], 0, 0, 0);
-  }
-#pragma unroll
-  for (int i = 0; i < 4; i++)
-#pragma unroll
-    for (int r = 0; r < 4; r++) {
-      float v = lsum[i][r];
-      v += __shfl_xor(v, 1, 64);
-      v += __shfl_xor(v, 2, 64);
-      v += __shfl_xor(v, 4, 64);
-      v += __shfl_xor(v, 8, 64);
-      lsum[i][r] = 1.0f / v;
-    }
-#pragma unroll
-  for (int i = 0; i < 4; i++)
-#pragma unroll
-    for (int r = 0; r < 4; r++) {
-      int lq = i * 16 + quad * 4 + r;
-      if (lq < 49) {
-        int iy = lq / 7, ix = lq - iy * 7;
-        int n = (wy * 7 + iy) * 56 + wx * 7 + ix;
-        bf16* op = O + ((size_t)(b * 3136 + n)) * 128 + h * 32;
-        op[l15]      = __float2bfloat16(acc[i][0][r] * lsum[i][r]);
-        op[16 + l15] = __float2bfloat16(acc[i][1][r] * lsum[i][r]);
-      }
-    }
 }
 
 extern "C" void kernel_launch(void* const* d_in, const int* in_sizes, int n_in,
@@ -674,12 +661,12 @@
   bf16*  xb  = (bf16*)ob;
   bf16*  Q12 = (bf16*)(ob + szBNC);
   bf16*  L1  = (bf16*)ws;
-  float* X1Ppart = (float*)ws;
+  bf16*  X1  = (bf16*)ws;
+  bf16*  L2  = (bf16*)(ws + szBNC);
+  float* X1Ppart = (float*)(ws + 2 * szBNC);
+  bf16*  X2  = (bf16*)(ws + 2 * szBNC);
   bf16*  X1N = (bf16*)ob;
   bf16*  KV1 = (bf16*)(ob + 8388608);
-  bf16*  X1  = (bf16*)ws;
-  bf16*  L2  = (bf16*)(ws + szBNC);
-  bf16*  X2  = (bf16*)(ws + 2 * szBNC);
   char*  wtb = ws + 2 * szBNC + szBNh;
   bf16* wT_x    = (bf16*)(wtb);
   bf16* wT_kv1  = (bf16*)(wtb + 393216);
@@ -692,15 +679,14 @@
       x, xb, sr_w, lepe_lin_w, kv2_w, q1_w, q2_w, kv1_w, proj_w,
       wT_sr, wT_x, wT_kv1, wT_proj, srbase);
 
-  gemm_x3<<<4704, 256, 0, stream>>>(xb, wT_x, lepe_lin_b, L1, KV2, Q12);
-
-  dwconv8_kernel<<<12544, 256, 0, stream>>>(L1, lepe_conv_w, lepe_conv_b, L2);
-
-  attn2_mfma<<<dim3(64, 32), 256, 0, stream>>>(Q12, KV2, X2);
-
-  gemm_sr<<<dim3(2, 49, 8), 256, 0, stream>>>(xb, wT_sr, srbase, X1Ppart);
-  ln_gelu_kernel<<<6272, 256, 0, stream>>>(X1Ppart, sr_b, norm_g, norm_b, X1N);
-  gemm_kv1<<<dim3(2, 49), 256, 0, stream>>>(X1N, wT_kv1, KV1);
+  gemm_x3sr<<<5096, 256, 0, stream>>>(
+      xb, wT_x, lepe_lin_b, L1, KV2, Q12, wT_sr, srbase, X1Ppart);
+
+  dwln_kernel<<<18816, 256, 0, stream>>>(
+      L1, lepe_conv_w, lepe_conv_b, X1Ppart, sr_b, norm_g, norm_b, L2, X1N);
+
+  attn2kv1_kernel<<<2146, 256, 0, stream>>>(Q12, KV2, X1N, wT_kv1, X2, KV1);
+
   attn1_mfma<<<dim3(13, 4, 32), 256, 0, stream>>>(Q12, KV1, X1);
 
   gemm_proj_mfma<<<1568, 256, 0, stream>>>(
```
